# Kernel optimization log

Hardware: AMD Instinct MI355X
Metric: run time of the kernel (lower is better)

The kernel has to match this reference:

```python
import jax, jax.numpy as jnp
import numpy as np

VOCAB = 50257
EMBED_DIM = 1024
FRONT_DIM = 2048  # int(embed_dim * front_embed_mul)
BATCH, SEQ = 4, 4096


def setup_inputs() -> dict:
    key = jax.random.key(0)
    k_idx, k_emb, k_w1, k_b1, k_w2, k_b2 = jax.random.split(key, 6)
    idxs = jax.random.randint(k_idx, (BATCH, SEQ), 0, VOCAB, dtype=jnp.int64)
    tok_embed = jax.random.normal(k_emb, (VOCAB, FRONT_DIM), dtype=jnp.float32)
    # torch nn.Linear weights are [out, in]
    W1 = jax.random.normal(k_w1, (EMBED_DIM, FRONT_DIM), dtype=jnp.float32) * (1.0 / np.sqrt(FRONT_DIM))
    b1 = jax.random.normal(k_b1, (EMBED_DIM,), dtype=jnp.float32) * 0.01
    W2 = jax.random.normal(k_w2, (EMBED_DIM, EMBED_DIM), dtype=jnp.float32) * (1.0 / np.sqrt(EMBED_DIM))
    b2 = jax.random.normal(k_b2, (EMBED_DIM,), dtype=jnp.float32) * 0.01
    return {"idxs": idxs, "tok_embed": tok_embed, "W1": W1, "b1": b1, "W2": W2, "b2": b2}


def reference(idxs, tok_embed, W1, b1, W2, b2):
    # Embedding gather: [B, S, front_dim]
    x = tok_embed[idxs]
    # integration1: Linear(front_dim -> embed_dim)
    x = jnp.einsum('bsf,ef->bse', x, W1) + b1
    # exact (erf-based) GELU, matching torch F.gelu default
    x = jax.nn.gelu(x, approximate=False)
    # integration2: Linear(embed_dim -> embed_dim)
    x = jnp.einsum('bse,oe->bso', x, W2) + b2
    return x
```

## Files before the change

### kernel.cpp

```cpp
#include <hip/hip_runtime.h>
#include <hip/hip_bf16.h>

typedef __attribute__((ext_vector_type(4))) float floatx4;
typedef __attribute__((ext_vector_type(8))) short short8;
typedef __attribute__((ext_vector_type(8))) unsigned short ushortx8;

#define K1 2048
#define N1 1024

__device__ __forceinline__ unsigned short f2bf(float f) {
  __hip_bfloat16 h = __float2bfloat16(f);
  return __builtin_bit_cast(unsigned short, h);
}

__device__ __forceinline__ void gload_lds16(const void* g, void* l) {
  __builtin_amdgcn_global_load_lds(
      (__attribute__((address_space(1))) void*)const_cast<void*>(g),
      (__attribute__((address_space(3))) void*)l, 16, 0, 0);
}

__global__ void cvt_bf16_kernel(const float* __restrict__ src,
                                unsigned short* __restrict__ dst, int n4) {
  int i = blockIdx.x * blockDim.x + threadIdx.x;
  if (i >= n4) return;
  float4 f = reinterpret_cast<const float4*>(src)[i];
  ushort4 o;
  o.x = f2bf(f.x); o.y = f2bf(f.y); o.z = f2bf(f.z); o.w = f2bf(f.w);
  reinterpret_cast<ushort4*>(dst)[i] = o;
}

__global__ __launch_bounds__(256) void gather_cvt_kernel(
    const int* __restrict__ idxs, const float* __restrict__ tok,
    unsigned short* __restrict__ xb) {
  const int row = blockIdx.x;
  const float* src = tok + (size_t)idxs[row] * K1;
  unsigned short* dst = xb + (size_t)row * K1;
  const int o = threadIdx.x * 8;
  const float4 f0 = *reinterpret_cast<const float4*>(src + o);
  const float4 f1 = *reinterpret_cast<const float4*>(src + o + 4);
  ushortx8 u;
  u[0] = f2bf(f0.x); u[1] = f2bf(f0.y); u[2] = f2bf(f0.z); u[3] = f2bf(f0.w);
  u[4] = f2bf(f1.x); u[5] = f2bf(f1.y); u[6] = f2bf(f1.z); u[7] = f2bf(f1.w);
  *reinterpret_cast<ushortx8*>(dst + o) = u;
}

template <int KDIM, int EPI>
__global__ __launch_bounds__(512, 2) void gemm256_kernel(
    const unsigned short* __restrict__ A, const unsigned short* __restrict__ Bw,
    const float* __restrict__ bias, void* __restrict__ outp) {
  __shared__ unsigned short Asub[2][16384];
  __shared__ unsigned short Bsub[2][16384];
  const int t = threadIdx.x;
  const int p = blockIdx.x;
  const int bid = (p & 7) * 32 + (p >> 3);
  const int bm = bid >> 2, bn = bid & 3;
  const int brow0 = bm * 256, bcol0 = bn * 256;
  const int lane = t & 63, w = t >> 6;
  const int wm = w >> 2, wn = w & 3;
  const int fr = lane & 15, kg2 = lane >> 4;

  const int srow = t >> 3;
  const int cg = (t & 7) ^ (srow & 7);
  const unsigned short* aq[4];
  const unsigned short* bq[4];
#pragma unroll
  for (int q = 0; q < 4; ++q) {
    aq[q] = A + (size_t)(brow0 + srow + 64 * q) * KDIM + cg * 8;
    bq[q] = Bw + (size_t)(bcol0 + srow + 64 * q) * KDIM + cg * 8;
  }
  const int t8 = t * 8;

  const int arow_sh = (wm * 128 + fr) * 64;
  const int brow_sh = (wn * 64 + fr) * 64;

  floatx4 acc[8][4] = {};
  constexpr int NT = KDIM / 64;

  auto stage = [&](int d, int k0) {
#pragma unroll
    for (int q = 0; q < 4; ++q) {
      gload_lds16(aq[q] + k0, &Asub[d][t8 + q * 4096]);
      gload_lds16(bq[q] + k0, &Bsub[d][t8 + q * 4096]);
    }
  };
  auto compute = [&](int cur) {
#pragma unroll
    for (int ks = 0; ks < 2; ++ks) {
      const int sl = ((ks * 4 + kg2) ^ (fr & 7)) * 8;
      short8 bf[4];
#pragma unroll
      for (int j = 0; j < 4; ++j)
        bf[j] = *reinterpret_cast<const short8*>(&Bsub[cur][brow_sh + j * 1024 + sl]);
#pragma unroll
      for (int i = 0; i < 8; ++i) {
        const short8 af = *reinterpret_cast<const short8*>(&Asub[cur][arow_sh + i * 1024 + sl]);
#pragma unroll
        for (int j = 0; j < 4; ++j)
          acc[i][j] = __builtin_amdgcn_mfma_f32_16x16x32_bf16(af, bf[j], acc[i][j], 0, 0, 0);
      }
    }
  };

  stage(0, 0);
#pragma unroll 1
  for (int it = 0; it < NT - 1; ++it) {
    const int cur = it & 1;
    stage(cur ^ 1, (it + 1) * 64);
    asm volatile("s_waitcnt vmcnt(8)\ns_barrier" ::: "memory");
    compute(cur);
    asm volatile("s_waitcnt lgkmcnt(0)\ns_barrier" ::: "memory");
  }
  asm volatile("s_waitcnt vmcnt(0)\ns_barrier" ::: "memory");
  compute((NT - 1) & 1);

  const int er0 = brow0 + wm * 128 + kg2 * 4;
  const int ec0 = bcol0 + wn * 64 + fr;
  if constexpr (EPI == 0) {
    unsigned short* hout = (unsigned short*)outp;
#pragma unroll
    for (int j = 0; j < 4; ++j) {
      const float bv = bias[ec0 + j * 16];
#pragma unroll
      for (int i = 0; i < 8; ++i)
#pragma unroll
        for (int r = 0; r < 4; ++r) {
          float v = acc[i][j][r] + bv;
          v = 0.5f * v * (1.0f + erff(v * 0.70710678118654752f));
          hout[(size_t)(er0 + i * 16 + r) * N1 + (ec0 + j * 16)] = f2bf(v);
        }
    }
  } else {
    float* fout = (float*)outp;
#pragma unroll
    for (int j = 0; j < 4; ++j) {
      const float bv = bias[ec0 + j * 16];
#pragma unroll
      for (int i = 0; i < 8; ++i)
#pragma unroll
        for (int r = 0; r < 4; ++r)
          fout[(size_t)(er0 + i * 16 + r) * N1 + (ec0 + j * 16)] = acc[i][j][r] + bv;
    }
  }
}

extern "C" void kernel_launch(void* const* d_in, const int* in_sizes, int n_in,
                              void* d_out, int out_size, void* d_ws, size_t ws_size,
                              hipStream_t stream) {
  const int* idxs = (const int*)d_in[0];
  const float* tok = (const float*)d_in[1];
  const float* W1 = (const float*)d_in[2];
  const float* b1 = (const float*)d_in[3];
  const float* W2 = (const float*)d_in[4];
  const float* b2 = (const float*)d_in[5];
  float* out = (float*)d_out;

  unsigned short* W1b = (unsigned short*)d_ws;
  unsigned short* W2b = (unsigned short*)((char*)d_ws + (4u << 20));
  unsigned short* xb = (unsigned short*)((char*)d_ws + (6u << 20));
  unsigned short* hbuf = (unsigned short*)((char*)d_ws + (70u << 20));

  cvt_bf16_kernel<<<2048, 256, 0, stream>>>(W1, W1b, 524288);
  cvt_bf16_kernel<<<1024, 256, 0, stream>>>(W2, W2b, 262144);
  gather_cvt_kernel<<<16384, 256, 0, stream>>>(idxs, tok, xb);
  gemm256_kernel<2048, 0><<<256, 512, 0, stream>>>(xb, W1b, b1, hbuf);
  gemm256_kernel<1024, 1><<<256, 512, 0, stream>>>(hbuf, W2b, b2, out);
}
```

Measured before the change: 166.6 us.

## Interleave global-to-LDS loads with split MFMA phases and raise wave priority

The GEMM main loop is restructured so that the next tile's four global-to-LDS load pairs are issued one at a time between four smaller MFMA phases, rather than all at once before the compute. Each phase loads its A fragments from LDS, waits only for those, and runs its 16 MFMAs under s_setprio(1), pinned in place with sched_barriers. The aim is to spread memory issue across compute and keep the matrix units busier. In exchange, each iteration now has four barriers instead of two, which adds synchronisation overhead and makes the schedule more rigid.

New measurement: 194.4 us. +16.7%, slower.

```diff
diff --git a/kernel.cpp b/kernel.cpp
--- a/kernel.cpp
+++ b/kernel.cpp
@@ -1,5 +1,6 @@
 #include <hip/hip_runtime.h>
 #include <hip/hip_bf16.h>
+
 
 typedef __attribute__((ext_vector_type(4))) float floatx4;
 typedef __attribute__((ext_vector_type(8))) short short8;
@@ -76,42 +77,69 @@
   floatx4 acc[8][4] = {};
   constexpr int NT = KDIM / 64;
 
-  auto stage = [&](int d, int k0) {
-#pragma unroll
-    for (int q = 0; q < 4; ++q) {
-      gload_lds16(aq[q] + k0, &Asub[d][t8 + q * 4096]);
-      gload_lds16(bq[q] + k0, &Bsub[d][t8 + q * 4096]);
+#define ISSUE_PAIR(d, k0, P)                                   \
+  do {                                                         \
+    gload_lds16(aq[P] + (k0), &Asub[d][t8 + (P)*4096]);        \
+    gload_lds16(bq[P] + (k0), &Bsub[d][t8 + (P)*4096]);        \
+  } while (0)
+
+#define MFMA_PHASE(cur, KS, I0, LOADB)                                        \
+  do {                                                                        \
+    const int sl = (((KS)*4 + kg2) ^ (fr & 7)) * 8;                           \
+    short8 af0, af1, af2, af3;                                                \
+    if (LOADB) {                                                              \
+      bf[0] = *(const short8*)&Bsub[cur][brow_sh + 0 * 1024 + sl];            \
+      bf[1] = *(const short8*)&Bsub[cur][brow_sh + 1 * 1024 + sl];            \
+      bf[2] = *(const short8*)&Bsub[cur][brow_sh + 2 * 1024 + sl];            \
+      bf[3] = *(const short8*)&Bsub[cur][brow_sh + 3 * 1024 + sl];            \
+    }                                                                         \
+    af0 = *(const short8*)&Asub[cur][arow_sh + ((I0) + 0) * 1024 + sl];       \
+    af1 = *(const short8*)&Asub[cur][arow_sh + ((I0) + 1) * 1024 + sl];       \
+    af2 = *(const short8*)&Asub[cur][arow_sh + ((I0) + 2) * 1024 + sl];       \
+    af3 = *(const short8*)&Asub[cur][arow_sh + ((I0) + 3) * 1024 + sl];       \
+    asm volatile("s_waitcnt lgkmcnt(0)" ::: "memory");                        \
+    __builtin_amdgcn_sched_barrier(0);                                        \
+    __builtin_amdgcn_s_setprio(1);                                            \
+    _Pragma("unroll") for (int j = 0; j < 4; ++j) {                           \
+      acc[(I0) + 0][j] = __builtin_amdgcn_mfma_f32_16x16x32_bf16(af0, bf[j], acc[(I0) + 0][j], 0, 0, 0); \
+      acc[(I0) + 1][j] = __builtin_amdgcn_mfma_f32_16x16x32_bf16(af1, bf[j], acc[(I0) + 1][j], 0, 0, 0); \
+      acc[(I0) + 2][j] = __builtin_amdgcn_mfma_f32_16x16x32_bf16(af2, bf[j], acc[(I0) + 2][j], 0, 0, 0); \
+      acc[(I0) + 3][j] = __builtin_amdgcn_mfma_f32_16x16x32_bf16(af3, bf[j], acc[(I0) + 3][j], 0, 0, 0); \
+    }                                                                         \
+    __builtin_amdgcn_s_setprio(0);                                            \
+    __builtin_amdgcn_sched_barrier(0);                                        \
+    asm volatile("s_barrier" ::: "memory");                                   \
+  } while (0)
+
+  ISSUE_PAIR(0, 0, 0);
+  ISSUE_PAIR(0, 0, 1);
+  ISSUE_PAIR(0, 0, 2);
+  ISSUE_PAIR(0, 0, 3);
+
+#pragma unroll 1
+  for (int tt = 0; tt < NT; ++tt) {
+    const int cur = tt & 1;
+    const int nbuf = cur ^ 1;
+    const int nk = (tt + 1) * 64;
+    if (tt + 1 < NT) {
+      ISSUE_PAIR(nbuf, nk, 0);
+      asm volatile("s_waitcnt vmcnt(2)" ::: "memory");
+    } else {
+      asm volatile("s_waitcnt vmcnt(0)" ::: "memory");
     }
-  };
-  auto compute = [&](int cur) {
-#pragma unroll
-    for (int ks = 0; ks < 2; ++ks) {
-      const int sl = ((ks * 4 + kg2) ^ (fr & 7)) * 8;
-      short8 bf[4];
-#pragma unroll
-      for (int j = 0; j < 4; ++j)
-        bf[j] = *reinterpret_cast<const short8*>(&Bsub[cur][brow_sh + j * 1024 + sl]);
-#pragma unroll
-      for (int i = 0; i < 8; ++i) {
-        const short8 af = *reinterpret_cast<const short8*>(&Asub[cur][arow_sh + i * 1024 + sl]);
-#pragma unroll
-        for (int j = 0; j < 4; ++j)
-          acc[i][j] = __builtin_amdgcn_mfma_f32_16x16x32_bf16(af, bf[j], acc[i][j], 0, 0, 0);
-      }
-    }
-  };
+    asm volatile("s_barrier" ::: "memory");
 
-  stage(0, 0);
-#pragma unroll 1
-  for (int it = 0; it < NT - 1; ++it) {
-    const int cur = it & 1;
-    stage(cur ^ 1, (it + 1) * 64);
-    asm volatile("s_waitcnt vmcnt(8)\ns_barrier" ::: "memory");
-    compute(cur);
-    asm volatile("s_waitcnt lgkmcnt(0)\ns_barrier" ::: "memory");
+    short8 bf[4];
+    if (tt + 1 < NT) ISSUE_PAIR(nbuf, nk, 1);
+    MFMA_PHASE(cur, 0, 0, true);
+    if (tt + 1 < NT) ISSUE_PAIR(nbuf, nk, 2);
+    MFMA_PHASE(cur, 0, 4, false);
+    if (tt + 1 < NT) ISSUE_PAIR(nbuf, nk, 3);
+    MFMA_PHASE(cur, 1, 0, true);
+    MFMA_PHASE(cur, 1, 4, false);
   }
-  asm volatile("s_waitcnt vmcnt(0)\ns_barrier" ::: "memory");
-  compute((NT - 1) & 1);
+#undef MFMA_PHASE
+#undef ISSUE_PAIR
 
   const int er0 = brow0 + wm * 128 + kg2 * 4;
   const int ec0 = bcol0 + wn * 64 + fr;
```

## Fuse embedding gather and bf16 conversion into first GEMM's A-tile loading

Applied to the files above, without the earlier changes.

Removes the separate gather+convert kernel and its bf16 intermediate buffer; the first GEMM now loads fp32 embedding rows directly via registers, converts to bf16, and writes to LDS while overlapping with MFMA compute. B tiles still use direct global-to-LDS loads, and MFMA sections get a raised wave priority. This saves a full write and read of the activation matrix but doubles A-tile read bytes per block and adds register pressure and load latency inside the GEMM loop.

After: 155.5 us. -6.7%, faster.

```diff
diff --git a/kernel.cpp b/kernel.cpp
--- a/kernel.cpp
+++ b/kernel.cpp
@@ -7,6 +7,8 @@
 
 #define K1 2048
 #define N1 1024
+#define K2 1024
+#define N2 1024
 
 __device__ __forceinline__ unsigned short f2bf(float f) {
   __hip_bfloat16 h = __float2bfloat16(f);
@@ -29,25 +31,10 @@
   reinterpret_cast<ushort4*>(dst)[i] = o;
 }
 
-__global__ __launch_bounds__(256) void gather_cvt_kernel(
+__global__ __launch_bounds__(512, 2) void gemm1_fused_kernel(
     const int* __restrict__ idxs, const float* __restrict__ tok,
-    unsigned short* __restrict__ xb) {
-  const int row = blockIdx.x;
-  const float* src = tok + (size_t)idxs[row] * K1;
-  unsigned short* dst = xb + (size_t)row * K1;
-  const int o = threadIdx.x * 8;
-  const float4 f0 = *reinterpret_cast<const float4*>(src + o);
-  const float4 f1 = *reinterpret_cast<const float4*>(src + o + 4);
-  ushortx8 u;
-  u[0] = f2bf(f0.x); u[1] = f2bf(f0.y); u[2] = f2bf(f0.z); u[3] = f2bf(f0.w);
-  u[4] = f2bf(f1.x); u[5] = f2bf(f1.y); u[6] = f2bf(f1.z); u[7] = f2bf(f1.w);
-  *reinterpret_cast<ushortx8*>(dst + o) = u;
-}
-
-template <int KDIM, int EPI>
-__global__ __launch_bounds__(512, 2) void gemm256_kernel(
-    const unsigned short* __restrict__ A, const unsigned short* __restrict__ Bw,
-    const float* __restrict__ bias, void* __restrict__ outp) {
+    const unsigned short* __restrict__ W1b, const float* __restrict__ b1,
+    unsigned short* __restrict__ hout) {
   __shared__ unsigned short Asub[2][16384];
   __shared__ unsigned short Bsub[2][16384];
   const int t = threadIdx.x;
@@ -61,12 +48,119 @@
 
   const int srow = t >> 3;
   const int cg = (t & 7) ^ (srow & 7);
+  const float* aqf[4];
+  const unsigned short* bq[4];
+#pragma unroll
+  for (int q = 0; q < 4; ++q) {
+    const int ridx = idxs[brow0 + srow + 64 * q];
+    aqf[q] = tok + (size_t)ridx * K1 + cg * 8;
+    bq[q] = W1b + (size_t)(bcol0 + srow + 64 * q) * K1 + cg * 8;
+  }
+  const int t8 = t * 8;
+
+  floatx4 acc[8][4] = {};
+  constexpr int NT = K1 / 64;
+
+  float4 av[4][2];
+  auto loadA = [&](int k0) {
+#pragma unroll
+    for (int q = 0; q < 4; ++q) {
+      av[q][0] = *reinterpret_cast<const float4*>(aqf[q] + k0);
+      av[q][1] = *reinterpret_cast<const float4*>(aqf[q] + k0 + 4);
+    }
+  };
+  auto writeA = [&](int d) {
+#pragma unroll
+    for (int q = 0; q < 4; ++q) {
+      ushortx8 u;
+      u[0] = f2bf(av[q][0].x); u[1] = f2bf(av[q][0].y);
+      u[2] = f2bf(av[q][0].z); u[3] = f2bf(av[q][0].w);
+      u[4] = f2bf(av[q][1].x); u[5] = f2bf(av[q][1].y);
+      u[6] = f2bf(av[q][1].z); u[7] = f2bf(av[q][1].w);
+      *reinterpret_cast<ushortx8*>(&Asub[d][t8 + q * 4096]) = u;
+    }
+  };
+  auto issueB = [&](int d, int k0) {
+#pragma unroll
+    for (int q = 0; q < 4; ++q)
+      gload_lds16(bq[q] + k0, &Bsub[d][t8 + q * 4096]);
+  };
+  auto computeKS = [&](int cur, int ks) {
+    const int sl = ((ks * 4 + kg2) ^ (fr & 7)) * 8;
+    short8 bf[4];
+#pragma unroll
+    for (int j = 0; j < 4; ++j)
+      bf[j] = *(const short8*)&Bsub[cur][(wn * 64 + j * 16 + fr) * 64 + sl];
+    __builtin_amdgcn_s_setprio(1);
+#pragma unroll
+    for (int i = 0; i < 8; ++i) {
+      const short8 af = *(const short8*)&Asub[cur][(wm * 128 + i * 16 + fr) * 64 + sl];
+#pragma unroll
+      for (int j = 0; j < 4; ++j)
+        acc[i][j] = __builtin_amdgcn_mfma_f32_16x16x32_bf16(af, bf[j], acc[i][j], 0, 0, 0);
+    }
+    __builtin_amdgcn_s_setprio(0);
+  };
+
+  loadA(0);
+  issueB(0, 0);
+  writeA(0);
+  asm volatile("s_waitcnt vmcnt(0) lgkmcnt(0)\ns_barrier" ::: "memory");
+
+#pragma unroll 1
+  for (int tt = 0; tt < NT; ++tt) {
+    const int cur = tt & 1;
+    const int nbuf = cur ^ 1;
+    const bool pf = (tt + 1 < NT);
+    const int nk = (tt + 1) * 64;
+    if (pf) {
+      loadA(nk);
+      issueB(nbuf, nk);
+    }
+    computeKS(cur, 0);
+    if (pf) writeA(nbuf);
+    computeKS(cur, 1);
+    asm volatile("s_waitcnt vmcnt(0) lgkmcnt(0)\ns_barrier" ::: "memory");
+  }
+
+  const int er0 = brow0 + wm * 128 + kg2 * 4;
+  const int ec0 = bcol0 + wn * 64 + fr;
+#pragma unroll
+  for (int j = 0; j < 4; ++j) {
+    const float bv = b1[ec0 + j * 16];
+#pragma unroll
+    for (int i = 0; i < 8; ++i)
+#pragma unroll
+      for (int r = 0; r < 4; ++r) {
+        float v = acc[i][j][r] + bv;
+        v = 0.5f * v * (1.0f + erff(v * 0.70710678118654752f));
+        hout[(size_t)(er0 + i * 16 + r) * N1 + (ec0 + j * 16)] = f2bf(v);
+      }
+  }
+}
+
+__global__ __launch_bounds__(512, 2) void gemm2_kernel(
+    const unsigned short* __restrict__ A, const unsigned short* __restrict__ Bw,
+    const float* __restrict__ bias, float* __restrict__ out) {
+  __shared__ unsigned short Asub[2][16384];
+  __shared__ unsigned short Bsub[2][16384];
+  const int t = threadIdx.x;
+  const int p = blockIdx.x;
+  const int bid = (p & 7) * 32 + (p >> 3);
+  const int bm = bid >> 2, bn = bid & 3;
+  const int brow0 = bm * 256, bcol0 = bn * 256;
+  const int lane = t & 63, w = t >> 6;
+  const int wm = w >> 2, wn = w & 3;
+  const int fr = lane & 15, kg2 = lane >> 4;
+
+  const int srow = t >> 3;
+  const int cg = (t & 7) ^ (srow & 7);
   const unsigned short* aq[4];
   const unsigned short* bq[4];
 #pragma unroll
   for (int q = 0; q < 4; ++q) {
-    aq[q] = A + (size_t)(brow0 + srow + 64 * q) * KDIM + cg * 8;
-    bq[q] = Bw + (size_t)(bcol0 + srow + 64 * q) * KDIM + cg * 8;
+    aq[q] = A + (size_t)(brow0 + srow + 64 * q) * K2 + cg * 8;
+    bq[q] = Bw + (size_t)(bcol0 + srow + 64 * q) * K2 + cg * 8;
   }
   const int t8 = t * 8;
 
@@ -74,7 +168,7 @@
   const int brow_sh = (wn * 64 + fr) * 64;
 
   floatx4 acc[8][4] = {};
-  constexpr int NT = KDIM / 64;
+  constexpr int NT = K2 / 64;
 
   auto stage = [&](int d, int k0) {
 #pragma unroll
@@ -115,31 +209,14 @@
 
   const int er0 = brow0 + wm * 128 + kg2 * 4;
   const int ec0 = bcol0 + wn * 64 + fr;
-  if constexpr (EPI == 0) {
-    unsigned short* hout = (unsigned short*)outp;
-#pragma unroll
-    for (int j = 0; j < 4; ++j) {
-      const float bv = bias[ec0 + j * 16];
-#pragma unroll
-      for (int i = 0; i < 8; ++i)
-#pragma unroll
-        for (int r = 0; r < 4; ++r) {
-          float v = acc[i][j][r] + bv;
-          v = 0.5f * v * (1.0f + erff(v * 0.70710678118654752f));
-          hout[(size_t)(er0 + i * 16 + r) * N1 + (ec0 + j * 16)] = f2bf(v);
-        }
-    }
-  } else {
-    float* fout = (float*)outp;
-#pragma unroll
-    for (int j = 0; j < 4; ++j) {
-      const float bv = bias[ec0 + j * 16];
-#pragma unroll
-      for (int i = 0; i < 8; ++i)
-#pragma unroll
-        for (int r = 0; r < 4; ++r)
-          fout[(size_t)(er0 + i * 16 + r) * N1 + (ec0 + j * 16)] = acc[i][j][r] + bv;
-    }
+#pragma unroll
+  for (int j = 0; j < 4; ++j) {
+    const float bv = bias[ec0 + j * 16];
+#pragma unroll
+    for (int i = 0; i < 8; ++i)
+#pragma unroll
+      for (int r = 0; r < 4; ++r)
+        out[(size_t)(er0 + i * 16 + r) * N2 + (ec0 + j * 16)] = acc[i][j][r] + bv;
   }
 }
 
@@ -156,12 +233,10 @@
 
   unsigned short* W1b = (unsigned short*)d_ws;
   unsigned short* W2b = (unsigned short*)((char*)d_ws + (4u << 20));
-  unsigned short* xb = (unsigned short*)((char*)d_ws + (6u << 20));
-  unsigned short* hbuf = (unsigned short*)((char*)d_ws + (70u << 20));
+  unsigned short* hbuf = (unsigned short*)((char*)d_ws + (6u << 20));
 
   cvt_bf16_kernel<<<2048, 256, 0, stream>>>(W1, W1b, 524288);
   cvt_bf16_kernel<<<1024, 256, 0, stream>>>(W2, W2b, 262144);
-  gather_cvt_kernel<<<16384, 256, 0, stream>>>(idxs, tok, xb);
-  gemm256_kernel<2048, 0><<<256, 512, 0, stream>>>(xb, W1b, b1, hbuf);
-  gemm256_kernel<1024, 1><<<256, 512, 0, stream>>>(hbuf, W2b, b2, out);
-}
+  gemm1_fused_kernel<<<256, 512, 0, stream>>>(idxs, tok, W1b, b1, hbuf);
+  gemm2_kernel<<<256, 512, 0, stream>>>(hbuf, W2b, b2, out);
+}
```
